# Kernel tuning notes

Measured on AMD Instinct MI355X. Metric: run time of the kernel, lower is better.

The kernel has to match this reference:

```python
import jax, jax.numpy as jnp
import numpy as np

B, T, C = 2, 2048, 2048
H = 16
HS = C // H           # 128
ROT = HS // 2         # 64 partial-rotary dims
BASE = 10000.0


def setup_inputs() -> dict:
    key = jax.random.key(0)
    ks = jax.random.split(key, 9)
    s = 1.0 / np.sqrt(C)
    return {
        "x": jax.random.normal(ks[0], (B, T, C), jnp.float32),
        "Wq": jax.random.normal(ks[1], (C, C), jnp.float32) * s,
        "bq": jax.random.normal(ks[2], (C,), jnp.float32) * 0.02,
        "Wk": jax.random.normal(ks[3], (C, C), jnp.float32) * s,
        "bk": jax.random.normal(ks[4], (C,), jnp.float32) * 0.02,
        "Wv": jax.random.normal(ks[5], (C, C), jnp.float32) * s,
        "bv": jax.random.normal(ks[6], (C,), jnp.float32) * 0.02,
        "Wo": jax.random.normal(ks[7], (C, C), jnp.float32) * s,
        "bo": jax.random.normal(ks[8], (C,), jnp.float32) * 0.02,
    }


def _rotate_half(u):
    u1, u2 = u[..., : u.shape[-1] // 2], u[..., u.shape[-1] // 2 :]
    return jnp.concatenate((-u2, u1), axis=-1)


def _rope_tables(t_len):
    inv_freq = 1.0 / (BASE ** (jnp.arange(0, ROT, 2, dtype=jnp.float32) / ROT))
    freqs = jnp.arange(t_len, dtype=jnp.float32)[:, None] * inv_freq[None, :]
    emb = jnp.concatenate((freqs, freqs), axis=-1)  # [T, ROT]
    return jnp.cos(emb), jnp.sin(emb)


def reference(x, Wq, bq, Wk, bk, Wv, bv, Wo, bo):
    Bs, Ts, Cs = x.shape
    q = (x @ Wq.T + bq).reshape(Bs, Ts, H, HS).transpose(0, 2, 1, 3)  # [B,H,T,HS]
    k = (x @ Wk.T + bk).reshape(Bs, Ts, H, HS).transpose(0, 2, 1, 3)
    v = (x @ Wv.T + bv).reshape(Bs, Ts, H, HS).transpose(0, 2, 1, 3)

    # partial rotary on first ROT dims of each head
    cos, sin = _rope_tables(Ts)  # [T, ROT] broadcast over B,H
    q_rot, q_pass = q[..., :ROT], q[..., ROT:]
    k_rot, k_pass = k[..., :ROT], k[..., ROT:]
    q_rot = q_rot * cos + _rotate_half(q_rot) * sin
    k_rot = k_rot * cos + _rotate_half(k_rot) * sin
    q = jnp.concatenate((q_rot, q_pass), axis=-1)
    k = jnp.concatenate((k_rot, k_pass), axis=-1)

    att = jnp.einsum("bhqd,bhkd->bhqk", q, k) * (1.0 / np.sqrt(HS))
    causal = jnp.tril(jnp.ones((Ts, Ts), dtype=bool))
    att = jnp.where(causal, att, jnp.float32(-jnp.inf))
    att = jax.nn.softmax(att, axis=-1)
    out = jnp.einsum("bhqk,bhkd->bhqd", att, v)          # [B,H,T,HS]
    out = out.transpose(0, 2, 1, 3).reshape(Bs, Ts, Cs)  # [B,T,C]
    return out @ Wo.T + bo
```

## Files before the change

### kernel.cpp

```cpp
#include <hip/hip_runtime.h>
#include <hip/hip_bf16.h>

#define Bdim 2
#define Tdim 2048
#define Cdim 2048
#define Hn   16

using bf16x8 = __attribute__((ext_vector_type(8))) short;
using f32x4  = __attribute__((ext_vector_type(4))) float;
using f32x16 = __attribute__((ext_vector_type(16))) float;
typedef __hip_bfloat16 bf16;

#define VMWAIT(n) asm volatile("s_waitcnt vmcnt(" #n ")" ::: "memory")
#define CROW(r, hi) (((r) & 3) + 8 * ((r) >> 2) + 4 * (hi))
#define QS2 ((float)(0.08838834764831845 * 1.4426950408889634))
#define THR2 11.5415603f

__device__ __forceinline__ void load_lds16(const void* g, void* l) {
  __builtin_amdgcn_global_load_lds(
      (const __attribute__((address_space(1))) void*)g,
      (__attribute__((address_space(3))) void*)l, 16, 0, 0);
}

__device__ __forceinline__ float bf2f(unsigned short u) {
  union { unsigned int i; float f; } x; x.i = ((unsigned int)u) << 16; return x.f;
}
__device__ __forceinline__ unsigned short f2bf(float f) {
  bf16 h = __float2bfloat16(f); return *(unsigned short*)&h;
}
__device__ __forceinline__ unsigned cvtpk(float lo, float hi) {
  unsigned r;
  asm volatile("v_cvt_pk_bf16_f32 %0, %1, %2" : "=v"(r) : "v"(lo), "v"(hi));
  return r;
}

__global__ __launch_bounds__(256) void cvt_all(const float* __restrict__ x,
                                               const float* __restrict__ w0,
                                               const float* __restrict__ w1,
                                               const float* __restrict__ w2,
                                               const float* __restrict__ w3,
                                               bf16* __restrict__ dx,
                                               bf16* __restrict__ d0,
                                               bf16* __restrict__ d1,
                                               bf16* __restrict__ d2,
                                               bf16* __restrict__ d3) {
  const int NX = (Bdim * Tdim * Cdim) / 4;
  const int NW = (Cdim * Cdim) / 4;
  int i = blockIdx.x * 256 + threadIdx.x;
  int stride = gridDim.x * 256;
  for (; i < NX + 4 * NW; i += stride) {
    const float* s; bf16* d; int j;
    if (i < NX) { s = x; d = dx; j = i; }
    else {
      int k = i - NX;
      int wsel = k >> 20;
      j = k & (NW - 1);
      s = wsel == 0 ? w0 : wsel == 1 ? w1 : wsel == 2 ? w2 : w3;
      d = wsel == 0 ? d0 : wsel == 1 ? d1 : wsel == 2 ? d2 : d3;
    }
    float4 v = ((const float4*)s)[j];
    ushort4 o;
    o.x = f2bf(v.x); o.y = f2bf(v.y); o.z = f2bf(v.z); o.w = f2bf(v.w);
    ((ushort4*)d)[j] = o;
  }
}

__global__ __launch_bounds__(256) void rope_tables_k(float2* __restrict__ cst) {
  int idx = blockIdx.x * blockDim.x + threadIdx.x;
  if (idx >= Tdim * 32) return;
  int t = idx >> 5, i = idx & 31;
  double f = pow(10000.0, -(double)i / 32.0);
  double ang = (double)t * f;
  cst[idx] = make_float2((float)cos(ang), (float)sin(ang));
}

__global__ __launch_bounds__(512, 2) void gemmQKV(
    const bf16* __restrict__ A, const bf16* __restrict__ Wcat,
    const float* __restrict__ b0, const float* __restrict__ b1, const float* __restrict__ b2,
    bf16* __restrict__ oq, bf16* __restrict__ ok, bf16* __restrict__ vt,
    const float2* __restrict__ cst) {
  extern __shared__ char lds[];
  const int tid = threadIdx.x, lane = tid & 63, wid = tid >> 6;
  const int l31 = lane & 31, hi = lane >> 5;
  const int wr = wid >> 2, wc = wid & 3;
  const int wbase = wid * 1024;

  const int q8 = gridDim.x >> 3;
  const int swz = ((int)blockIdx.x & 7) * q8 + ((int)blockIdx.x >> 3);
  const int bm = (swz >> 4) * 256;
  const int strip = swz & 15;

  const int rS = tid >> 2, sS = tid & 3;
  const int ssw = (sS ^ ((rS >> 1) & 3)) << 3;
  const bf16* thrA = A + (size_t)(bm + rS) * 2048 + ssw;
  const bf16* thrB = Wcat + (size_t)(strip * 384 + rS) * 2048 + ssw;

#define SA(T, DB) { load_lds16(thrA + (T) * 32, (DB) + wbase);                              \
                    load_lds16(thrA + (size_t)128 * 2048 + (T) * 32, (DB) + 8192 + wbase); }
#define SB(T, DB) { load_lds16(thrB + (T) * 32, (DB) + 16384 + wbase);                      \
                    load_lds16(thrB + (size_t)128 * 2048 + (T) * 32, (DB) + 24576 + wbase); \
                    load_lds16(thrB + (size_t)256 * 2048 + (T) * 32, (DB) + 32768 + wbase); }

  f32x16 acc[4][3] = {};
  bf16x8 afr[4], bfr[3];
  const int q2 = (l31 >> 1) & 3;
  const int aoff = (wr * 128 + l31) * 64;
  const int boff = 16384 + (wc * 96 + l31) * 64;
  const int sl0 = (hi ^ q2) << 4;
  const int sl1 = sl0 ^ 32;

#define READF(PB, SL)                                                        \
  {                                                                          \
    const char* _p = (PB);                                                   \
    _Pragma("unroll")                                                        \
    for (int m_ = 0; m_ < 4; ++m_)                                           \
      afr[m_] = *(const bf16x8*)(_p + aoff + m_ * 2048 + (SL));              \
    _Pragma("unroll")                                                        \
    for (int n_ = 0; n_ < 3; ++n_)                                           \
      bfr[n_] = *(const bf16x8*)(_p + boff + n_ * 2048 + (SL));              \
  }

#define MF12()                                                               \
  __builtin_amdgcn_s_setprio(1);                                             \
  _Pragma("unroll")                                                          \
  for (int m_ = 0; m_ < 4; ++m_)                                             \
    _Pragma("unroll")                                                        \
    for (int n_ = 0; n_ < 3; ++n_)                                           \
      acc[m_][n_] = __builtin_amdgcn_mfma_f32_32x32x16_bf16(                 \
          afr[m_], bfr[n_], acc[m_][n_], 0, 0, 0);                           \
  __builtin_amdgcn_s_setprio(0);

  SA(0, lds); SB(0, lds);
  SA(1, lds + 40960); SB(1, lds + 40960);
  VMWAIT(5);
  __builtin_amdgcn_s_barrier();
  __builtin_amdgcn_sched_barrier(0);
  READF(lds, sl0);

  const char* rb = lds;
  const char* nb = lds + 40960;
  char* sb = lds + 81920;
  const int NT = 64;

  for (int t = 0; t < NT - 2; ++t) {
    MF12();
    READF(rb, sl1);
    MF12();
    VMWAIT(0);
    __builtin_amdgcn_s_barrier();
    __builtin_amdgcn_sched_barrier(0);
    SA(t + 2, sb); SB(t + 2, sb);
    READF(nb, sl0);
    char* old = (char*)rb; rb = nb; nb = sb; sb = old;
  }
  {
    MF12();
    READF(rb, sl1);
    MF12();
    VMWAIT(0);
    __builtin_amdgcn_s_barrier();
    __builtin_amdgcn_sched_barrier(0);
    READF(nb, sl0);
    rb = nb;
  }
  {
    MF12();
    READF(rb, sl1);
    MF12();
  }

  __syncthreads();
  if (wc == 3) {
    const int col0 = strip * 384 + 288;
    const int mat = col0 >> 11;
    if (mat < 2) {
      const int oc0 = col0 & 2047;
      const float bv = (mat == 0 ? b0 : b1)[oc0 + l31];
      #pragma unroll
      for (int m = 0; m < 4; ++m)
        #pragma unroll
        for (int g = 0; g < 4; ++g) {
          f32x4 v;
          v[0] = acc[m][0][4 * g + 0] + bv;
          v[1] = acc[m][0][4 * g + 1] + bv;
          v[2] = acc[m][0][4 * g + 2] + bv;
          v[3] = acc[m][0][4 * g + 3] + bv;
          *(f32x4*)(lds + (((((wr * 4 + m) * 4 + g) * 2 + hi) * 32) + l31) * 16) = v;
        }
    }
  }
  __syncthreads();

  #pragma unroll
  for (int m = 0; m < 4; ++m) {
    const int rowb = bm + wr * 128 + m * 32;
    const int bb = rowb >> 11, tb = rowb & 2047;
    #pragma unroll
    for (int n = 0; n < 3; ++n) {
      const int col0 = strip * 384 + wc * 96 + n * 32;
      const int mat = col0 >> 11;
      const int oc0 = col0 & 2047;
      const float bv = (mat == 0 ? b0 : mat == 1 ? b1 : b2)[oc0 + l31];
      if (mat == 2) {
        const int hh = oc0 >> 7;
        bf16* dst = vt + ((size_t)((bb * 16 + hh) * 128 + (oc0 & 127) + l31)) * 2048 + tb;
        #pragma unroll
        for (int g = 0; g < 4; ++g) {
          ushort4 pk;
          pk.x = f2bf(acc[m][n][4 * g + 0] + bv);
          pk.y = f2bf(acc[m][n][4 * g + 1] + bv);
          pk.z = f2bf(acc[m][n][4 * g + 2] + bv);
          pk.w = f2bf(acc[m][n][4 * g + 3] + bv);
          *(ushort4*)(dst + g * 8 + hi * 4) = pk;
        }
      } else {
        const float qs = (mat == 0) ? QS2 : 1.0f;
        bf16* obf = (mat == 0) ? oq : ok;
        const int hb = (wc * 3 + n) & 3;
        if (hb == 0) {
          if (wc == 2 && n == 2) {
            #pragma unroll
            for (int g = 0; g < 4; ++g) {
              f32x4 ux = *(const f32x4*)(lds + (((((wr * 4 + m) * 4 + g) * 2 + hi) * 32) + l31) * 16);
              #pragma unroll
              for (int j = 0; j < 4; ++j) {
                const int r = 4 * g + j;
                const int row = rowb + j + 8 * g + 4 * hi;
                const int tt = row & 2047;
                float2 cs = cst[tt * 32 + l31];
                float u0 = acc[m][n][r] + bv;
                float u1 = ux[j];
                obf[(size_t)row * 2048 + oc0 + l31] =
                    __float2bfloat16((u0 * cs.x - u1 * cs.y) * qs);
                obf[(size_t)row * 2048 + oc0 + 32 + l31] =
                    __float2bfloat16((u1 * cs.x + u0 * cs.y) * qs);
              }
            }
          } else {
            const float bv1 = (mat == 0 ? b0 : b1)[oc0 + 32 + l31];
            #pragma unroll
            for (int r = 0; r < 16; ++r) {
              const int row = rowb + (r & 3) + 8 * (r >> 2) + 4 * hi;
              const int tt = row & 2047;
              float2 cs = cst[tt * 32 + l31];
              float u0 = acc[m][n][r] + bv;
              float u1 = acc[m][n + 1][r] + bv1;
              obf[(size_t)row * 2048 + oc0 + l31] =
                  __float2bfloat16((u0 * cs.x - u1 * cs.y) * qs);
              obf[(size_t)row * 2048 + oc0 + 32 + l31] =
                  __float2bfloat16((u1 * cs.x + u0 * cs.y) * qs);
            }
          }
        } else if (hb >= 2) {
          #pragma unroll
          for (int r = 0; r < 16; ++r) {
            const int row = rowb + (r & 3) + 8 * (r >> 2) + 4 * hi;
            obf[(size_t)row * 2048 + oc0 + l31] =
                __float2bfloat16((acc[m][n][r] + bv) * qs);
          }
        }
      }
    }
  }
#undef SA
#undef SB
#undef READF
#undef MF12
}

__global__ __launch_bounds__(512, 2) void gemmWo(
    const bf16* __restrict__ A, const bf16* __restrict__ W0,
    const float* __restrict__ b0, float* __restrict__ out, int K, int nby) {
  extern __shared__ char lds[];
  const int tid = threadIdx.x, lane = tid & 63, wid = tid >> 6;
  const int l15 = lane & 15, lhi = lane >> 4;
  const int wr = wid >> 2, wc = wid & 3;
  const int fb = (wc & 1) | ((wc >> 1) << 2);

  const int q8 = gridDim.x >> 3;
  const int swz = ((int)blockIdx.x & 7) * q8 + ((int)blockIdx.x >> 3);
  const int bm = (swz / nby) * 128, bn = (swz % nby) * 256;
  const bf16* Asrc = A + (size_t)bm * K;
  const bf16* Wsrc = W0 + (size_t)bn * K;

  const bf16 *sA0, *sA1, *sB00, *sB01, *sB10, *sB11;
  {
    int c = tid, r = c >> 3, sl = c & 7;
    size_t off = (size_t)r * K + ((sl ^ (r & 7)) << 3);
    sA0 = Asrc + off;
    sA1 = Asrc + (size_t)64 * K + off;
    sB00 = Wsrc + off;
    sB10 = Wsrc + (size_t)128 * K + off;
  }
  {
    int c = 512 + tid, r = c >> 3, sl = c & 7;
    size_t off = (size_t)r * K + ((sl ^ (r & 7)) << 3);
    sB01 = Wsrc + off;
    sB11 = Wsrc + (size_t)128 * K + off;
  }
  const int ldsA = wid * 1024;

#define SA0(t) load_lds16(sA0 + (t) * 64, lds + ((t) & 1) * 49152 + ldsA)
#define SA1(t) load_lds16(sA1 + (t) * 64, lds + ((t) & 1) * 49152 + 8192 + ldsA)
#define SB0(t) { load_lds16(sB00 + (t) * 64, lds + ((t) & 1) * 49152 + 16384 + ldsA); \
                 load_lds16(sB01 + (t) * 64, lds + ((t) & 1) * 49152 + 24576 + ldsA); }
#define SB1(t) { load_lds16(sB10 + (t) * 64, lds + ((t) & 1) * 49152 + 32768 + ldsA); \
                 load_lds16(sB11 + (t) * 64, lds + ((t) & 1) * 49152 + 40960 + ldsA); }

  f32x4 acc[4][4] = {};
  const int NT = K / 64;
  const int NI = NT / 2;
  const int asw = (l15 & 7) << 4;
  bf16x8 afr[2][2], bfr0[2][2], bfr1[2][2];

#define READ_A(BASE)                                                            \
  _Pragma("unroll")                                                             \
  for (int ii = 0; ii < 2; ++ii)                                                \
    _Pragma("unroll")                                                           \
    for (int kk = 0; kk < 2; ++kk)                                              \
      afr[ii][kk] = *(const bf16x8*)((BASE) + (wr * 32 + ii * 16 + l15) * 128   \
                                     + ((kk * 64 + lhi * 16) ^ asw));

#define READ_B(BASE, DST)                                                       \
  _Pragma("unroll")                                                             \
  for (int j = 0; j < 2; ++j)                                                   \
    _Pragma("unroll")                                                           \
    for (int kk = 0; kk < 2; ++kk)                                              \
      DST[j][kk] = *(const bf16x8*)((BASE) + ((fb + 2 * j) * 16 + l15) * 128    \
                                    + ((kk * 64 + lhi * 16) ^ asw));

#define MFMA_Q(MH, NH, BF)                                                      \
  __builtin_amdgcn_s_setprio(1);                                                \
  _Pragma("unroll")                                                             \
  for (int ii = 0; ii < 2; ++ii)                                                \
    _Pragma("unroll")                                                           \
    for (int j = 0; j < 2; ++j)                                                 \
      _Pragma("unroll")                                                         \
      for (int kk = 0; kk < 2; ++kk)                                            \
        acc[(MH) * 2 + ii][(NH) * 2 + j] =                                      \
            __builtin_amdgcn_mfma_f32_16x16x32_bf16(                            \
                afr[ii][kk], BF[j][kk], acc[(MH) * 2 + ii][(NH) * 2 + j], 0, 0, 0); \
  __builtin_amdgcn_s_setprio(0);

#define BAR_IN()                                                                \
  __builtin_amdgcn_s_barrier();                                                 \
  asm volatile("s_waitcnt lgkmcnt(0)" ::: "memory");                            \
  __builtin_amdgcn_sched_barrier(0);

#define BAR_OUT() __builtin_amdgcn_s_barrier();

  SA0(0); SB0(0); SB1(0); SA1(0);
  SA0(1); SB0(1); SB1(1);
  VMWAIT(5);
  __builtin_amdgcn_s_barrier();

  char* const buf0 = lds;
  char* const buf1 = lds + 49152;

  for (int i = 0; i < NI; ++i) {
    const int t0 = 2 * i, t1 = t0 + 1;
    const bool lastI = (i == NI - 1);

    READ_A(buf0);
    READ_B(buf0 + 16384, bfr0);
    SA1(t1);
    BAR_IN(); MFMA_Q(0, 0, bfr0); BAR_OUT();

    READ_B(buf0 + 32768, bfr1);
    if (!lastI) SA0(t0 + 2);
    BAR_IN(); MFMA_Q(0, 1, bfr1); BAR_OUT();

    READ_A(buf0 + 8192);
    if (!lastI) SB0(t0 + 2);
    BAR_IN(); MFMA_Q(1, 0, bfr0); BAR_OUT();

    if (!lastI) { SB1(t0 + 2); VMWAIT(5); } else VMWAIT(0);
    BAR_IN(); MFMA_Q(1, 1, bfr1); BAR_OUT();

    READ_A(buf1);
    READ_B(buf1 + 16384, bfr0);
    if (!lastI) SA1(t0 + 2);
    BAR_IN(); MFMA_Q(0, 0, bfr0); BAR_OUT();

    READ_B(buf1 + 32768, bfr1);
    if (!lastI) SA0(t1 + 2);
    BAR_IN(); MFMA_Q(0, 1, bfr1); BAR_OUT();

    READ_A(buf1 + 8192);
    if (!lastI) SB0(t1 + 2);
    BAR_IN(); MFMA_Q(1, 0, bfr0); BAR_OUT();

    if (!lastI) { SB1(t1 + 2); VMWAIT(5); }
    BAR_IN(); MFMA_Q(1, 1, bfr1); BAR_OUT();
  }

  #pragma unroll
  for (int mi = 0; mi < 4; ++mi) {
    const int row = bm + (mi >> 1) * 64 + wr * 32 + (mi & 1) * 16 + lhi * 4;
    #pragma unroll
    for (int nj = 0; nj < 4; ++nj) {
      const int col = bn + (nj >> 1) * 128 + (fb + 2 * (nj & 1)) * 16 + l15;
      const float bv = b0[col];
      #pragma unroll
      for (int r = 0; r < 4; ++r)
        out[(size_t)(row + r) * 2048 + col] = acc[mi][nj][r] + bv;
    }
  }
#undef SA0
#undef SA1
#undef SB0
#undef SB1
#undef READ_A
#undef READ_B
#undef MFMA_Q
#undef BAR_IN
#undef BAR_OUT
}

__global__ __launch_bounds__(256, 2) void attn_kernel(const bf16* __restrict__ Q,
                                                      const bf16* __restrict__ Kb,
                                                      const bf16* __restrict__ Vt,
                                                      bf16* __restrict__ O) {
  extern __shared__ char lds[];
  const int tid = threadIdx.x, lane = tid & 63, wave = tid >> 6;
  const int l31 = lane & 31, hi = lane >> 5;
  const int hi16 = hi << 4;

  const int bid = blockIdx.x;
  const int half = bid >> 8;
  const int idx = bid & 255;
  const int g = idx >> 5;
  const int qt = half ? g : (15 - g);
  const int bh = idx & 31;
  const int b = bh >> 4, h = bh & 15;
  const size_t bT = (size_t)b * Tdim;

  const int qb = qt * 128 + wave * 32;
  const int myq = qb + l31;

  bf16x8 qf[8];
  {
    const bf16* qrow = Q + (bT + myq) * Cdim + h * 128;
    #pragma unroll
    for (int ds = 0; ds < 8; ++ds)
      qf[ds] = *(const bf16x8*)(qrow + ds * 16 + hi * 8);
  }

  auto stageKV = [&](int kt) {
    const int k0 = kt * 64;
    char* kb = lds + (kt & 1) * 16384;
    char* vb = lds + 32768 + (kt & 1) * 16384;
    #pragma unroll
    for (int i = 0; i < 4; ++i) {
      int cb = i * 256 + wave * 64;
      int c = cb + lane;
      {
        int row = c >> 4, slot = c & 15;
        load_lds16(Kb + (bT + k0 + row) * Cdim + h * 128 + ((slot ^ (row & 7)) << 3),
                   kb + cb * 16);
      }
      {
        int row = c >> 3, slot = c & 7;
        load_lds16(Vt + ((size_t)(bh * 128 + row)) * Tdim + k0 + ((slot ^ (row & 7)) << 3),
                   vb + cb * 16);
      }
    }
  };

  f32x16 o[4] = {};
  float mrun = -1e30f, lrun = 0.f;

  const int nt = 2 * (qt + 1);
  stageKV(0);

  for (int kt = 0; kt < nt; ++kt) {
    if (kt + 1 < nt) { stageKV(kt + 1); VMWAIT(8); } else { VMWAIT(0); }
    __syncthreads();
    const char* kbuf = lds + (kt & 1) * 16384;
    const char* vbuf = lds + 32768 + (kt & 1) * 16384;
    const int k0 = kt * 64;

    const bool active = (k0 <= qb + 31);
    if (active) {
      f32x16 s0 = {}, s1 = {};
      const int krow0 = l31, krow1 = 32 + l31;
      const int ksw = (l31 & 7) << 4;
      __builtin_amdgcn_s_setprio(1);
      #pragma unroll
      for (int ds = 0; ds < 8; ++ds) {
        const int boff = (ds * 32 + hi16) ^ ksw;
        bf16x8 kf0 = *(const bf16x8*)(kbuf + krow0 * 256 + boff);
        bf16x8 kf1 = *(const bf16x8*)(kbuf + krow1 * 256 + boff);
        s0 = __builtin_amdgcn_mfma_f32_32x32x16_bf16(kf0, qf[ds], s0, 0, 0, 0);
        s1 = __builtin_amdgcn_mfma_f32_32x32x16_bf16(kf1, qf[ds], s1, 0, 0, 0);
      }
      __builtin_amdgcn_s_setprio(0);

      if (k0 + 63 > qb) {
        #pragma unroll
        for (int r = 0; r < 16; ++r) {
          const int key = k0 + CROW(r, hi);
          if (key > myq)      s0[r] = -1e30f;
          if (key + 32 > myq) s1[r] = -1e30f;
        }
      }

      float mx = s0[0];
      #pragma unroll
      for (int r = 1; r < 16; ++r) mx = fmaxf(mx, s0[r]);
      #pragma unroll
      for (int r = 0; r < 16; ++r) mx = fmaxf(mx, s1[r]);
      mx = fmaxf(mx, __shfl_xor(mx, 32));
      if (!__all(mx <= mrun + THR2)) {
        const float mnew = fmaxf(mrun, mx);
        const float scl = __builtin_amdgcn_exp2f(mrun - mnew);
        lrun *= scl;
        #pragma unroll
        for (int r = 0; r < 16; ++r) {
          const float sr = __shfl(scl, CROW(r, hi));
          o[0][r] *= sr; o[1][r] *= sr; o[2][r] *= sr; o[3][r] *= sr;
        }
        mrun = mnew;
      }
      float p0[16], p1[16];
      float ps = 0.f;
      #pragma unroll
      for (int r = 0; r < 16; ++r) {
        p0[r] = __builtin_amdgcn_exp2f(s0[r] - mrun); ps += p0[r];
        p1[r] = __builtin_amdgcn_exp2f(s1[r] - mrun); ps += p1[r];
      }
      ps += __shfl_xor(ps, 32);
      lrun += ps;

      unsigned u0[8], u1[8];
      #pragma unroll
      for (int gg = 0; gg < 4; ++gg) {
        u0[gg * 2 + 0] = cvtpk(p0[gg * 4 + 0], p0[gg * 4 + 1]);
        u0[gg * 2 + 1] = cvtpk(p0[gg * 4 + 2], p0[gg * 4 + 3]);
        u1[gg * 2 + 0] = cvtpk(p1[gg * 4 + 0], p1[gg * 4 + 1]);
        u1[gg * 2 + 1] = cvtpk(p1[gg * 4 + 2], p1[gg * 4 + 3]);
      }
      bf16x8 paf[4];
      #pragma unroll
      for (int s = 0; s < 2; ++s) {
        const unsigned* us = s ? u1 : u0;
        #pragma unroll
        for (int gp = 0; gp < 2; ++gp) {
          unsigned snd0 = hi ? us[4 * gp + 0] : us[4 * gp + 2];
          unsigned snd1 = hi ? us[4 * gp + 1] : us[4 * gp + 3];
          unsigned rcv0 = __shfl_xor((int)snd0, 32);
          unsigned rcv1 = __shfl_xor((int)snd1, 32);
          union { unsigned w[4]; bf16x8 v; } fr;
          if (hi == 0) {
            fr.w[0] = us[4 * gp + 0]; fr.w[1] = us[4 * gp + 1];
            fr.w[2] = rcv0;           fr.w[3] = rcv1;
          } else {
            fr.w[0] = rcv0;           fr.w[1] = rcv1;
            fr.w[2] = us[4 * gp + 2]; fr.w[3] = us[4 * gp + 3];
          }
          paf[s * 2 + gp] = fr.v;
        }
      }

      __builtin_amdgcn_s_setprio(1);
      #pragma unroll
      for (int dblk = 0; dblk < 4; ++dblk) {
        const int d = dblk * 32 + l31;
        const int vswz = (d & 7) << 4;
        #pragma unroll
        for (int ks = 0; ks < 4; ++ks) {
          bf16x8 vf = *(const bf16x8*)(vbuf + d * 128 + ((ks * 32 + hi16) ^ vswz));
          o[dblk] = __builtin_amdgcn_mfma_f32_32x32x16_bf16(paf[ks], vf, o[dblk], 0, 0, 0);
        }
      }
      __builtin_amdgcn_s_setprio(0);
    }
    __syncthreads();
  }

  const float inv = 1.f / lrun;
  #pragma unroll
  for (int r = 0; r < 16; ++r) {
    const float ir = __shfl(inv, CROW(r, hi));
    const int qrow = qb + CROW(r, hi);
    bf16* orow = O + (bT + qrow) * Cdim + h * 128;
    #pragma unroll
    for (int dblk = 0; dblk < 4; ++dblk)
      orow[dblk * 32 + l31] = __float2bfloat16(o[dblk][r] * ir);
  }
}

extern "C" void kernel_launch(void* const* d_in, const int* in_sizes, int n_in,
                              void* d_out, int out_size, void* d_ws, size_t ws_size,
                              hipStream_t stream) {
  const float* x  = (const float*)d_in[0];
  const float* Wq = (const float*)d_in[1];
  const float* bq = (const float*)d_in[2];
  const float* Wk = (const float*)d_in[3];
  const float* bk = (const float*)d_in[4];
  const float* Wv = (const float*)d_in[5];
  const float* bv = (const float*)d_in[6];
  const float* Wo = (const float*)d_in[7];
  const float* bo = (const float*)d_in[8];

  char* ws = (char*)d_ws;
  const size_t SZ_X  = (size_t)Bdim * Tdim * Cdim * 2;
  const size_t SZ_W  = (size_t)Cdim * Cdim * 2;
  bf16* x_bf  = (bf16*)(ws);
  bf16* Wq_bf = (bf16*)(ws + SZ_X);
  bf16* Wk_bf = (bf16*)(ws + SZ_X + SZ_W);
  bf16* Wv_bf = (bf16*)(ws + SZ_X + 2 * SZ_W);
  bf16* Wo_bf = (bf16*)(ws + SZ_X + 3 * SZ_W);
  bf16* q_bf  = (bf16*)(ws + SZ_X + 4 * SZ_W);
  bf16* k_bf  = (bf16*)(ws + 2 * SZ_X + 4 * SZ_W);
  bf16* v_t   = (bf16*)(ws + 3 * SZ_X + 4 * SZ_W);
  bf16* a_bf  = (bf16*)(ws + 4 * SZ_X + 4 * SZ_W);
  float2* cst = (float2*)(ws + 5 * SZ_X + 4 * SZ_W);

  const int K = Cdim;

  rope_tables_k<<<(Tdim * 32 + 255) / 256, 256, 0, stream>>>(cst);
  cvt_all<<<2048, 256, 0, stream>>>(x, Wq, Wk, Wv, Wo,
                                    x_bf, Wq_bf, Wk_bf, Wv_bf, Wo_bf);

  gemmQKV<<<256, 512, 122880, stream>>>(
      x_bf, Wq_bf, bq, bk, bv, q_bf, k_bf, v_t, cst);

  attn_kernel<<<512, 256, 65536, stream>>>(q_bf, k_bf, v_t, a_bf);

  gemmWo<<<256, 512, 98304, stream>>>(
      a_bf, Wo_bf, bo, (float*)d_out, K, 8);
}
```

Measured before the change: 231.3 us.

## Halve QKV GEMM block tile and switch to double-buffered 4-wave pipeline

```diff
diff --git a/kernel.cpp b/kernel.cpp
--- a/kernel.cpp
+++ b/kernel.cpp
@@ -74,7 +74,7 @@
   cst[idx] = make_float2((float)cos(ang), (float)sin(ang));
 }
 
-__global__ __launch_bounds__(512, 2) void gemmQKV(
+__global__ __launch_bounds__(256, 2) void gemmQKV(
     const bf16* __restrict__ A, const bf16* __restrict__ Wcat,
     const float* __restrict__ b0, const float* __restrict__ b1, const float* __restrict__ b2,
     bf16* __restrict__ oq, bf16* __restrict__ ok, bf16* __restrict__ vt,
@@ -82,24 +82,26 @@
   extern __shared__ char lds[];
   const int tid = threadIdx.x, lane = tid & 63, wid = tid >> 6;
   const int l31 = lane & 31, hi = lane >> 5;
-  const int wr = wid >> 2, wc = wid & 3;
+  const int wr = wid >> 1, wc = wid & 1;
   const int wbase = wid * 1024;
 
   const int q8 = gridDim.x >> 3;
   const int swz = ((int)blockIdx.x & 7) * q8 + ((int)blockIdx.x >> 3);
-  const int bm = (swz >> 4) * 256;
-  const int strip = swz & 15;
+  const int bm = (swz >> 5) * 256;
+  const int strip = swz & 31;
 
   const int rS = tid >> 2, sS = tid & 3;
   const int ssw = (sS ^ ((rS >> 1) & 3)) << 3;
   const bf16* thrA = A + (size_t)(bm + rS) * 2048 + ssw;
-  const bf16* thrB = Wcat + (size_t)(strip * 384 + rS) * 2048 + ssw;
+  const bf16* thrB = Wcat + (size_t)(strip * 192 + rS) * 2048 + ssw;
 
 #define SA(T, DB) { load_lds16(thrA + (T) * 32, (DB) + wbase);                              \
-                    load_lds16(thrA + (size_t)128 * 2048 + (T) * 32, (DB) + 8192 + wbase); }
+                    load_lds16(thrA + (size_t)64 * 2048 + (T) * 32, (DB) + 4096 + wbase);   \
+                    load_lds16(thrA + (size_t)128 * 2048 + (T) * 32, (DB) + 8192 + wbase);  \
+                    load_lds16(thrA + (size_t)192 * 2048 + (T) * 32, (DB) + 12288 + wbase); }
 #define SB(T, DB) { load_lds16(thrB + (T) * 32, (DB) + 16384 + wbase);                      \
-                    load_lds16(thrB + (size_t)128 * 2048 + (T) * 32, (DB) + 24576 + wbase); \
-                    load_lds16(thrB + (size_t)256 * 2048 + (T) * 32, (DB) + 32768 + wbase); }
+                    load_lds16(thrB + (size_t)64 * 2048 + (T) * 32, (DB) + 20480 + wbase);  \
+                    load_lds16(thrB + (size_t)128 * 2048 + (T) * 32, (DB) + 24576 + wbase); }
 
   f32x16 acc[4][3] = {};
   bf16x8 afr[4], bfr[3];
@@ -131,47 +133,30 @@
   __builtin_amdgcn_s_setprio(0);
 
   SA(0, lds); SB(0, lds);
-  SA(1, lds + 40960); SB(1, lds + 40960);
-  VMWAIT(5);
+  VMWAIT(0);
   __builtin_amdgcn_s_barrier();
   __builtin_amdgcn_sched_barrier(0);
   READF(lds, sl0);
 
-  const char* rb = lds;
-  const char* nb = lds + 40960;
-  char* sb = lds + 81920;
   const int NT = 64;
-
-  for (int t = 0; t < NT - 2; ++t) {
+  for (int t = 0; t < NT; ++t) {
+    char* bufC = lds + (t & 1) * 28672;
+    char* bufO = lds + ((t + 1) & 1) * 28672;
+    if (t + 1 < NT) { SA(t + 1, bufO); SB(t + 1, bufO); }
     MF12();
-    READF(rb, sl1);
+    READF(bufC, sl1);
     MF12();
-    VMWAIT(0);
-    __builtin_amdgcn_s_barrier();
-    __builtin_amdgcn_sched_barrier(0);
-    SA(t + 2, sb); SB(t + 2, sb);
-    READF(nb, sl0);
-    char* old = (char*)rb; rb = nb; nb = sb; sb = old;
-  }
-  {
-    MF12();
-    READF(rb, sl1);
-    MF12();
-    VMWAIT(0);
-    __builtin_amdgcn_s_barrier();
-    __builtin_amdgcn_sched_barrier(0);
-    READF(nb, sl0);
-    rb = nb;
-  }
-  {
-    MF12();
-    READF(rb, sl1);
-    MF12();
+    if (t + 1 < NT) {
+      VMWAIT(0);
+      __builtin_amdgcn_s_barrier();
+      __builtin_amdgcn_sched_barrier(0);
+      READF(bufO, sl0);
+    }
   }
 
   __syncthreads();
-  if (wc == 3) {
-    const int col0 = strip * 384 + 288;
+  if (wc == 1 && (strip & 1)) {
+    const int col0 = strip * 192 + 96;
     const int mat = col0 >> 11;
     if (mat < 2) {
       const int oc0 = col0 & 2047;
@@ -197,7 +182,7 @@
     const int bb = rowb >> 11, tb = rowb & 2047;
     #pragma unroll
     for (int n = 0; n < 3; ++n) {
-      const int col0 = strip * 384 + wc * 96 + n * 32;
+      const int col0 = strip * 192 + wc * 96 + n * 32;
       const int mat = col0 >> 11;
       const int oc0 = col0 & 2047;
       const float bv = (mat == 0 ? b0 : mat == 1 ? b1 : b2)[oc0 + l31];
@@ -216,9 +201,10 @@
       } else {
         const float qs = (mat == 0) ? QS2 : 1.0f;
         bf16* obf = (mat == 0) ? oq : ok;
-        const int hb = (wc * 3 + n) & 3;
+        const float* bp = (mat == 0) ? b0 : b1;
+        const int hb = (col0 >> 5) & 3;
         if (hb == 0) {
-          if (wc == 2 && n == 2) {
+          if (n == 2) {
             #pragma unroll
             for (int g = 0; g < 4; ++g) {
               f32x4 ux = *(const f32x4*)(lds + (((((wr * 4 + m) * 4 + g) * 2 + hi) * 32) + l31) * 16);
@@ -237,7 +223,7 @@
               }
             }
           } else {
-            const float bv1 = (mat == 0 ? b0 : b1)[oc0 + 32 + l31];
+            const float bv1 = bp[oc0 + 32 + l31];
             #pragma unroll
             for (int r = 0; r < 16; ++r) {
               const int row = rowb + (r & 3) + 8 * (r >> 2) + 4 * hi;
@@ -623,7 +609,7 @@
   cvt_all<<<2048, 256, 0, stream>>>(x, Wq, Wk, Wv, Wo,
                                     x_bf, Wq_bf, Wk_bf, Wv_bf, Wo_bf);
 
-  gemmQKV<<<256, 512, 122880, stream>>>(
+  gemmQKV<<<512, 256, 57344, stream>>>(
       x_bf, Wq_bf, bq, bk, bv, q_bf, k_bf, v_t, cst);
 
   attn_kernel<<<512, 256, 65536, stream>>>(q_bf, k_bf, v_t, a_bf);
```

New measurement: 236.2 us. 1.02x slower.
